# Optimization experiments

Hardware: AMD Instinct MI355X
Metric: run time of the kernel (lower is better)

## Reference

```python
import jax, jax.numpy as jnp
import numpy as np

N = 50000
E = 600000
DIN = 128
HID = 128
NG = 64


def _gat(x, src, dst, W, a_s, a_d, b, heads, dout, concat):
    # PyG GATConv (eval mode): per-head linear, edge attention logits,
    # segment softmax over destination nodes, weighted scatter-sum.
    n = x.shape[0]
    xp = (x @ W.T).reshape(n, heads, dout)                     # [n, H, D]
    e = jax.nn.leaky_relu(jnp.sum(xp * a_s, -1)[src] + jnp.sum(xp * a_d, -1)[dst], 0.2)  # [Etot, H]
    m = jax.ops.segment_max(e, dst, num_segments=n)
    ex = jnp.exp(e - m[dst])
    alpha = ex / jax.ops.segment_sum(ex, dst, num_segments=n)[dst]
    out = jax.ops.segment_sum(xp[src] * alpha[:, :, None], dst, num_segments=n)  # [n, H, D]
    out = out.reshape(n, heads * dout) if concat else out.mean(axis=1)
    return out + b


def _forward(x, edge_index, batch, Wi1, bi1, Wi2, bi2, Wg0, As0, Ad0, bg0, Wg1, As1, Ad1, bg1, Wg2, As2, Ad2, bg2, Wg3, As3, Ad3, bg3, We1, be1, We2, be2, Wc1, bc1, Wc2, bc2, Wc3, bc3):
    n = x.shape[0]
    loops = jnp.arange(n, dtype=edge_index.dtype)              # add_self_loops=True
    src = jnp.concatenate([edge_index[0], loops])
    dst = jnp.concatenate([edge_index[1], loops])
    # input_proj (dropout is a no-op in eval)
    h = jax.nn.relu(x @ Wi1.T + bi1) @ Wi2.T + bi2
    specs = [(Wg0, As0, Ad0, bg0, 8, 16, True),
             (Wg1, As1, Ad1, bg1, 8, 16, True),
             (Wg2, As2, Ad2, bg2, 8, 16, True),
             (Wg3, As3, Ad3, bg3, 1, 128, False)]
    for i, (W, a_s, a_d, b, hd, do, cc) in enumerate(specs):
        res = h
        h = jax.nn.elu(_gat(h, src, dst, W, a_s, a_d, b, hd, do, cc))
        if i > 0:
            h = h + res  # residual (dims always equal: 128)
    enh = h + (jax.nn.relu(h @ We1.T + be1) @ We2.T + be2)
    # per-graph mean / max / std (unbiased, ddof=1) pooling via segment reduces
    cnt = jax.ops.segment_sum(jnp.ones((n,), enh.dtype), batch, num_segments=NG)
    s = jax.ops.segment_sum(enh, batch, num_segments=NG)
    ss = jax.ops.segment_sum(enh * enh, batch, num_segments=NG)
    c = jnp.maximum(cnt, 1.0)[:, None]
    mean = s / c
    mx = jax.ops.segment_max(enh, batch, num_segments=NG)
    var = (ss - c * mean * mean) / jnp.maximum(cnt - 1.0, 1.0)[:, None]
    std = jnp.where(cnt[:, None] > 1.0, jnp.sqrt(jnp.maximum(var, 0.0)), 0.0)
    g = jnp.concatenate([mean, mx, std], axis=1)               # [NG, 3*HID]
    h1 = jax.nn.relu(g @ Wc1.T + bc1)
    h2 = jax.nn.relu(h1 @ Wc2.T + bc2)
    return h2 @ Wc3.T + bc3


def setup_inputs():
    ks = jax.random.split(jax.random.key(0), 32)

    def gl(k, o, i):
        return jax.random.normal(k, (o, i), jnp.float32) * jnp.sqrt(2.0 / (o + i))

    inp = {}
    inp["x"] = jax.random.normal(ks[0], (N, DIN), jnp.float32)
    inp["edge_index"] = jax.random.randint(ks[1], (2, E), 0, N, dtype=jnp.int32)
    inp["batch"] = jnp.sort(jax.random.randint(ks[2], (N,), 0, NG, dtype=jnp.int32))
    inp["Wi1"] = gl(ks[3], HID, DIN); inp["bi1"] = jnp.zeros((HID,), jnp.float32)
    inp["Wi2"] = gl(ks[4], HID, HID); inp["bi2"] = jnp.zeros((HID,), jnp.float32)
    for li in range(3):
        inp[f"Wg{li}"] = gl(ks[5 + li], HID, HID)
        inp[f"As{li}"] = jax.random.normal(ks[8 + li], (8, 16), jnp.float32) * 0.1
        inp[f"Ad{li}"] = jax.random.normal(ks[11 + li], (8, 16), jnp.float32) * 0.1
        inp[f"bg{li}"] = jnp.zeros((HID,), jnp.float32)
    inp["Wg3"] = gl(ks[14], HID, HID)
    inp["As3"] = jax.random.normal(ks[15], (1, HID), jnp.float32) * 0.1
    inp["Ad3"] = jax.random.normal(ks[16], (1, HID), jnp.float32) * 0.1
    inp["bg3"] = jnp.zeros((HID,), jnp.float32)
    inp["We1"] = gl(ks[17], HID, HID); inp["be1"] = jnp.zeros((HID,), jnp.float32)
    inp["We2"] = gl(ks[18], HID, HID); inp["be2"] = jnp.zeros((HID,), jnp.float32)
    inp["Wc1"] = gl(ks[19], HID, 3 * HID); inp["bc1"] = jnp.zeros((HID,), jnp.float32)
    inp["Wc2"] = gl(ks[20], HID // 2, HID); inp["bc2"] = jnp.zeros((HID // 2,), jnp.float32)
    inp["Wc3"] = gl(ks[21], 2, HID // 2); inp["bc3"] = jnp.zeros((2,), jnp.float32)
    return inp


def reference(x, edge_index, batch, Wi1, bi1, Wi2, bi2, Wg0, As0, Ad0, bg0, Wg1, As1, Ad1, bg1, Wg2, As2, Ad2, bg2, Wg3, As3, Ad3, bg3, We1, be1, We2, be2, Wc1, bc1, Wc2, bc2, Wc3, bc3):
    return _forward(x, edge_index, batch, Wi1, bi1, Wi2, bi2, Wg0, As0, Ad0, bg0, Wg1, As1, Ad1, bg1, Wg2, As2, Ad2, bg2, Wg3, As3, Ad3, bg3, We1, be1, We2, be2, Wc1, bc1, Wc2, bc2, Wc3, bc3)
```

## Files before the change

kernel.cpp:

```cpp
#include <hip/hip_runtime.h>
#include <hip/hip_fp16.h>
#include <cstddef>

typedef _Float16 f16;
typedef f16 f16x8 __attribute__((ext_vector_type(8)));
typedef float f32x4 __attribute__((ext_vector_type(4)));

__device__ __forceinline__ unsigned f2mono(float f){
  unsigned u = __float_as_uint(f);
  return (u & 0x80000000u) ? ~u : (u | 0x80000000u);
}
__device__ __forceinline__ float mono2f(unsigned u){
  return (u & 0x80000000u) ? __uint_as_float(u & 0x7fffffffu) : __uint_as_float(~u);
}

struct WPtrs { const float* w[8]; };
__global__ void k_wcast(WPtrs p, f16* __restrict__ Wh){
  int wi = blockIdx.y;
  const float* W = p.w[wi];
  f16* dst = Wh + (size_t)wi * 16384;
  int i = (blockIdx.x*256 + threadIdx.x) * 8;
  float4 v0 = *(const float4*)(W + i), v1 = *(const float4*)(W + i + 4);
  f16x8 h = {(f16)v0.x,(f16)v0.y,(f16)v0.z,(f16)v0.w,
             (f16)v1.x,(f16)v1.y,(f16)v1.z,(f16)v1.w};
  *(f16x8*)(dst + i) = h;
}

template<typename TIN, bool RES>
__global__ __launch_bounds__(256) void k_gemm2(
    const TIN* __restrict__ in, const f16* __restrict__ W1, const f16* __restrict__ W2,
    const float* __restrict__ b1, const float* __restrict__ b2,
    const float* __restrict__ res, float* __restrict__ outF, __half* __restrict__ outH, int n)
{
  constexpr int LDW = 130;
  __shared__ f16 Wl[128*LDW];
  __shared__ f16 Al[32*LDW];
  __shared__ f16 Ml[32*LDW];
  const int tid = threadIdx.x;
  const int r0 = blockIdx.x * 32;
#pragma unroll
  for (int i = 0; i < 8; i++){
    int u = tid + 256*i; int row = u >> 4, c8 = (u & 15) * 8;
    *(f16x8*)&Wl[row*LDW + c8] = *(const f16x8*)(W1 + (size_t)row*128 + c8);
  }
#pragma unroll
  for (int i = 0; i < 2; i++){
    int u = tid + 256*i; int row = u >> 4, c8 = (u & 15) * 8;
    int gr = r0 + row;
    f16x8 v = {};
    if (gr < n){
      if constexpr (__is_same(TIN, __half)){
        v = *(const f16x8*)((const f16*)in + (size_t)gr*128 + c8);
      } else {
        const float4* q = (const float4*)((const float*)in + (size_t)gr*128 + c8);
        float4 v0 = q[0], v1 = q[1];
        v = f16x8{(f16)v0.x,(f16)v0.y,(f16)v0.z,(f16)v0.w,
                  (f16)v1.x,(f16)v1.y,(f16)v1.z,(f16)v1.w};
      }
    }
    *(f16x8*)&Al[row*LDW + c8] = v;
  }
  __syncthreads();
  const int wv = tid >> 6, lane = tid & 63;
  const int l15 = lane & 15, quad = lane >> 4;
  f32x4 acc[2][2] = {};
  {
    const f16* Ab = &Al[l15*LDW + quad*8];
    const f16* Bb = &Wl[(wv*32 + l15)*LDW + quad*8];
#pragma unroll
    for (int kc = 0; kc < 4; kc++){
      f16x8 a0 = *(const f16x8*)(Ab + kc*32);
      f16x8 a1 = *(const f16x8*)(Ab + 16*LDW + kc*32);
#pragma unroll
      for (int nt = 0; nt < 2; nt++){
        f16x8 b = *(const f16x8*)(Bb + nt*16*LDW + kc*32);
        acc[0][nt] = __builtin_amdgcn_mfma_f32_16x16x32_f16(a0, b, acc[0][nt], 0, 0, 0);
        acc[1][nt] = __builtin_amdgcn_mfma_f32_16x16x32_f16(a1, b, acc[1][nt], 0, 0, 0);
      }
    }
  }
#pragma unroll
  for (int nt = 0; nt < 2; nt++){
    int col = wv*32 + nt*16 + l15;
    float bv = b1[col];
#pragma unroll
    for (int rh = 0; rh < 2; rh++)
#pragma unroll
      for (int reg = 0; reg < 4; reg++){
        int row = rh*16 + quad*4 + reg;
        Ml[row*LDW + col] = (f16)fmaxf(acc[rh][nt][reg] + bv, 0.f);
      }
  }
  __syncthreads();
#pragma unroll
  for (int i = 0; i < 8; i++){
    int u = tid + 256*i; int row = u >> 4, c8 = (u & 15) * 8;
    *(f16x8*)&Wl[row*LDW + c8] = *(const f16x8*)(W2 + (size_t)row*128 + c8);
  }
  __syncthreads();
  f32x4 acc2[2][2] = {};
  {
    const f16* Ab = &Ml[l15*LDW + quad*8];
    const f16* Bb = &Wl[(wv*32 + l15)*LDW + quad*8];
#pragma unroll
    for (int kc = 0; kc < 4; kc++){
      f16x8 a0 = *(const f16x8*)(Ab + kc*32);
      f16x8 a1 = *(const f16x8*)(Ab + 16*LDW + kc*32);
#pragma unroll
      for (int nt = 0; nt < 2; nt++){
        f16x8 b = *(const f16x8*)(Bb + nt*16*LDW + kc*32);
        acc2[0][nt] = __builtin_amdgcn_mfma_f32_16x16x32_f16(a0, b, acc2[0][nt], 0, 0, 0);
        acc2[1][nt] = __builtin_amdgcn_mfma_f32_16x16x32_f16(a1, b, acc2[1][nt], 0, 0, 0);
      }
    }
  }
  __syncthreads();
  float* Cf = (float*)Wl;
#pragma unroll
  for (int nt = 0; nt < 2; nt++){
    int col = wv*32 + nt*16 + l15;
    float bv = b2[col];
#pragma unroll
    for (int rh = 0; rh < 2; rh++)
#pragma unroll
      for (int reg = 0; reg < 4; reg++){
        int row = rh*16 + quad*4 + reg;
        Cf[row*132 + col] = acc2[rh][nt][reg] + bv;
      }
  }
  __syncthreads();
  if constexpr (RES){
#pragma unroll
    for (int i = 0; i < 4; i++){
      int u = tid + 256*i;
      int row = u >> 5, c4 = (u & 31) * 4;
      int gr = r0 + row;
      if (gr < n){
        float4 r4 = *(const float4*)(res + (size_t)gr*128 + c4);
        float4 v = *(float4*)&Cf[row*132 + c4];
        v.x += r4.x; v.y += r4.y; v.z += r4.z; v.w += r4.w;
        *(float4*)(outF + (size_t)gr*128 + c4) = v;
      }
    }
  } else {
#pragma unroll
    for (int i = 0; i < 2; i++){
      int u = tid + 256*i;
      int row = u >> 4, c8 = (u & 15) * 8;
      int gr = r0 + row;
      if (gr < n){
        float4 a = *(float4*)&Cf[row*132 + c8];
        float4 b = *(float4*)&Cf[row*132 + c8 + 4];
        f16x8 h = {(f16)a.x,(f16)a.y,(f16)a.z,(f16)a.w,
                   (f16)b.x,(f16)b.y,(f16)b.z,(f16)b.w};
        *(f16x8*)((f16*)outH + (size_t)gr*128 + c8) = h;
      }
    }
  }
}

template<int PREP>
__global__ __launch_bounds__(256) void k_gat_gemm(
    const __half* __restrict__ in, const f16* __restrict__ Wm,
    const float* __restrict__ As, const float* __restrict__ Ad,
    float* __restrict__ es, float* __restrict__ ed,
    __half* __restrict__ outH, int n)
{
  constexpr int LDW = 130;
  __shared__ f16 Wl[64*LDW];
  __shared__ f16 Al[32*LDW];
  const int tid = threadIdx.x;
  const int ch = blockIdx.x & 1;
  const int r0 = (blockIdx.x >> 1) * 32;
#pragma unroll
  for (int i = 0; i < 4; i++){
    int u = tid + 256*i; int row = u >> 4, c8 = (u & 15) * 8;
    *(f16x8*)&Wl[row*LDW + c8] = *(const f16x8*)(Wm + (size_t)(ch*64 + row)*128 + c8);
  }
#pragma unroll
  for (int i = 0; i < 2; i++){
    int u = tid + 256*i; int row = u >> 4, c8 = (u & 15) * 8;
    int gr = r0 + row;
    f16x8 v = {};
    if (gr < n) v = *(const f16x8*)((const f16*)in + (size_t)gr*128 + c8);
    *(f16x8*)&Al[row*LDW + c8] = v;
  }
  __syncthreads();
  const int wv = tid >> 6, lane = tid & 63;
  const int l15 = lane & 15, quad = lane >> 4;
  const int rh = wv & 1, cq = wv >> 1;
  f32x4 acc[2] = {};
  const f16* Ab = &Al[(rh*16 + l15)*LDW + quad*8];
  const f16* Bb = &Wl[(cq*32 + l15)*LDW + quad*8];
#pragma unroll
  for (int kc = 0; kc < 4; kc++){
    f16x8 a = *(const f16x8*)(Ab + kc*32);
#pragma unroll
    for (int nt = 0; nt < 2; nt++){
      f16x8 b = *(const f16x8*)(Bb + nt*16*LDW + kc*32);
      acc[nt] = __builtin_amdgcn_mfma_f32_16x16x32_f16(a, b, acc[nt], 0, 0, 0);
    }
  }
  if constexpr (PREP == 1){
#pragma unroll
    for (int nt = 0; nt < 2; nt++){
      int hh = ch*4 + cq*2 + nt;
      float as_ = As[hh*16 + l15], ad_ = Ad[hh*16 + l15];
#pragma unroll
      for (int reg = 0; reg < 4; reg++){
        float se = acc[nt][reg] * as_;
        float sd = acc[nt][reg] * ad_;
#pragma unroll
        for (int off = 1; off < 16; off <<= 1){
          se += __shfl_xor(se, off); sd += __shfl_xor(sd, off);
        }
        int gr = r0 + rh*16 + quad*4 + reg;
        if (l15 == 0 && gr < n){ es[gr*8 + hh] = se; ed[gr*8 + hh] = sd; }
      }
    }
  } else {
    float as_[2], ad_[2];
#pragma unroll
    for (int nt = 0; nt < 2; nt++){
      int col = ch*64 + cq*32 + nt*16 + l15;
      as_[nt] = As[col]; ad_[nt] = Ad[col];
    }
#pragma unroll
    for (int reg = 0; reg < 4; reg++){
      float se = acc[0][reg]*as_[0] + acc[1][reg]*as_[1];
      float sd = acc[0][reg]*ad_[0] + acc[1][reg]*ad_[1];
#pragma unroll
      for (int off = 1; off < 16; off <<= 1){
        se += __shfl_xor(se, off); sd += __shfl_xor(sd, off);
      }
      int gr = r0 + rh*16 + quad*4 + reg;
      if (l15 == 0 && gr < n){ atomicAdd(&es[gr], se); atomicAdd(&ed[gr], sd); }
    }
  }
  __syncthreads();
  f16* St = Al;
#pragma unroll
  for (int nt = 0; nt < 2; nt++){
    int c2 = cq*32 + nt*16 + l15;
#pragma unroll
    for (int reg = 0; reg < 4; reg++){
      int row = rh*16 + quad*4 + reg;
      St[row*72 + c2] = (f16)acc[nt][reg];
    }
  }
  __syncthreads();
  {
    int row = tid >> 3, c8 = (tid & 7) * 8;
    int gr = r0 + row;
    if (gr < n)
      *(f16x8*)((f16*)outH + (size_t)gr*128 + ch*64 + c8) = *(f16x8*)&St[row*72 + c8];
  }
}

__global__ void k_deg(const int* __restrict__ ei, int* __restrict__ deg, int E, int N){
  int t = blockIdx.x*blockDim.x + threadIdx.x;
  if (t >= E + N) return;
  int d = (t < E) ? ei[E + t] : (t - E);
  atomicAdd(&deg[d], 1);
}
__global__ void k_scan1(const int* __restrict__ deg, int* __restrict__ bsum, int N){
  __shared__ int sd[256];
  int i = blockIdx.x*256 + threadIdx.x;
  sd[threadIdx.x] = (i < N) ? deg[i] : 0;
  __syncthreads();
  for (int s = 128; s > 0; s >>= 1){
    if (threadIdx.x < s) sd[threadIdx.x] += sd[threadIdx.x + s];
    __syncthreads();
  }
  if (threadIdx.x == 0) bsum[blockIdx.x] = sd[0];
}
__global__ void k_scan2(const int* __restrict__ bsum, int* __restrict__ boff, int nb){
  __shared__ int sd[256];
  int t = threadIdx.x;
  int v = (t < nb) ? bsum[t] : 0;
  sd[t] = v;
  __syncthreads();
  for (int s = 1; s < 256; s <<= 1){
    int u = (t >= s) ? sd[t - s] : 0;
    __syncthreads();
    sd[t] += u;
    __syncthreads();
  }
  if (t < nb) boff[t] = sd[t] - v;
}
__global__ void k_scan3(const int* __restrict__ deg, const int* __restrict__ boff,
                        int* __restrict__ rowptr, int N){
  __shared__ int sd[256];
  int tid = threadIdx.x;
  int i = blockIdx.x*256 + tid;
  sd[tid] = (i < N) ? deg[i] : 0;
  __syncthreads();
  for (int s = 1; s < 256; s <<= 1){
    int t = (tid >= s) ? sd[tid - s] : 0;
    __syncthreads();
    sd[tid] += t;
    __syncthreads();
  }
  if (i < N) rowptr[i+1] = boff[blockIdx.x] + sd[tid];
  if (i == 0) rowptr[0] = 0;
}
__global__ void k_fill(const int* __restrict__ ei, const int* __restrict__ rowptr,
                       int* __restrict__ fil, int* __restrict__ csr, int E, int N){
  int t = blockIdx.x*blockDim.x + threadIdx.x;
  if (t >= E + N) return;
  int s, d;
  if (t < E){ s = ei[t]; d = ei[E + t]; } else { s = d = t - E; }
  int pos = rowptr[d] + atomicAdd(&fil[d], 1);
  csr[pos] = s;
}

template<int H, int D>
__global__ __launch_bounds__(256) void k_aggregate(
    const __half* __restrict__ xp, const float* __restrict__ es, const float* __restrict__ ed,
    const int* __restrict__ rowptr, const int* __restrict__ csr,
    const float* __restrict__ bg, const float* res,
    float* out, __half* __restrict__ outH, int N)
{
  int gw = (blockIdx.x*256 + threadIdx.x) >> 6;
  if (gw >= N) return;
  const int lane = threadIdx.x & 63;
  const int j0 = lane*2;
  const int h0 = (H == 8) ? (lane >> 3) : 0;
  const int k8 = lane & 7;
  int beg = rowptr[gw], end = rowptr[gw+1];
  float edv = ed[gw*H + h0];
  float den = 0.f, a0 = 0.f, a1 = 0.f;
  int idx = beg + k8; if (idx >= end) idx = end - 1;
  int sE = csr[idx];
  float ev = es[sE*H + h0];
  for (int t = beg; t < end; t += 8){
    int nb = end - t; if (nb > 8) nb = 8;
    int sE_c = sE; float ev_c = ev;
    int tn = t + 8;
    if (tn < end){
      int idxn = tn + k8; if (idxn >= end) idxn = end - 1;
      sE = csr[idxn];
      ev = es[sE*H + h0];
    }
    float e = ev_c + edv;
    e = e > 0.f ? e : 0.2f*e;
    if (k8 >= nb) e = -1e30f;
    float w = __expf(e);
    float wk[8]; int sk[8];
#pragma unroll
    for (int k = 0; k < 8; k++){
      wk[k] = __shfl(w, (h0 << 3) + k);
      sk[k] = __shfl(sE_c, k);
    }
    float2 f[8];
#pragma unroll
    for (int k = 0; k < 8; k++)
      f[k] = __half22float2(*(const __half2*)(xp + (size_t)sk[k]*128 + j0));
#pragma unroll
    for (int k = 0; k < 8; k++){
      den += wk[k]; a0 += wk[k]*f[k].x; a1 += wk[k]*f[k].y;
    }
  }
  float inv = 1.f / den;
  float o0 = a0*inv + bg[j0];
  float o1 = a1*inv + bg[j0+1];
  o0 = o0 > 0.f ? o0 : __expf(o0) - 1.f;
  o1 = o1 > 0.f ? o1 : __expf(o1) - 1.f;
  if (res){ o0 += res[(size_t)gw*128 + j0]; o1 += res[(size_t)gw*128 + j0 + 1]; }
  *(float2*)(out + (size_t)gw*128 + j0) = make_float2(o0, o1);
  *(__half2*)(outH + (size_t)gw*128 + j0) = __floats2half2_rn(o0, o1);
}

__global__ __launch_bounds__(128) void k_pool(const float* __restrict__ enh,
    const int* __restrict__ batch, float* __restrict__ Ps, float* __restrict__ Pss,
    unsigned* __restrict__ Pmx, float* __restrict__ Pcnt, int N)
{
  int tid = threadIdx.x;
  int n0 = blockIdx.x * 32;
  if (n0 >= N) return;
  int n1 = min(n0 + 32, N);
  int cur = batch[n0];
  float sum = 0.f, ssq = 0.f, mx = -1e30f, cnt = 0.f;
  auto flush = [&](int b){
    atomicAdd(&Ps[b*128 + tid], sum);
    atomicAdd(&Pss[b*128 + tid], ssq);
    atomicMax(&Pmx[b*128 + tid], f2mono(mx));
    if (tid == 0) atomicAdd(&Pcnt[b], cnt);
  };
  for (int i = n0; i < n1; i++){
    int b = batch[i];
    if (b != cur){ flush(cur); cur = b; sum = 0.f; ssq = 0.f; mx = -1e30f; cnt = 0.f; }
    float v = enh[(size_t)i*128 + tid];
    sum += v; ssq += v*v; mx = fmaxf(mx, v); cnt += 1.f;
  }
  flush(cur);
}

__global__ void k_poolcls(const float* __restrict__ Ps, const float* __restrict__ Pss,
    const unsigned* __restrict__ Pmx, const float* __restrict__ Pcnt,
    const float* __restrict__ Wc1, const float* __restrict__ bc1,
    const float* __restrict__ Wc2, const float* __restrict__ bc2,
    const float* __restrict__ Wc3, const float* __restrict__ bc3,
    float* __restrict__ out)
{
  __shared__ float gs[384];
  __shared__ float hs[128];
  __shared__ float h2[64];
  int b = blockIdx.x, j = threadIdx.x;
  float cnt = Pcnt[b];
  float c = fmaxf(cnt, 1.f);
  float mean = Ps[b*128 + j] / c;
  float var = (Pss[b*128 + j] - c*mean*mean) / fmaxf(cnt - 1.f, 1.f);
  float sd = (cnt > 1.f) ? sqrtf(fmaxf(var, 0.f)) : 0.f;
  gs[j] = mean; gs[128 + j] = mono2f(Pmx[b*128 + j]); gs[256 + j] = sd;
  __syncthreads();
  float acc = bc1[j];
  const float4* wr = (const float4*)(Wc1 + (size_t)j*384);
  for (int i = 0; i < 96; i++){
    float4 w = wr[i];
    acc += gs[i*4]*w.x + gs[i*4+1]*w.y + gs[i*4+2]*w.z + gs[i*4+3]*w.w;
  }
  hs[j] = fmaxf(acc, 0.f);
  __syncthreads();
  if (j < 64){
    float a2 = bc2[j];
    const float4* w2 = (const float4*)(Wc2 + (size_t)j*128);
    for (int i = 0; i < 32; i++){
      float4 w = w2[i];
      a2 += hs[i*4]*w.x + hs[i*4+1]*w.y + hs[i*4+2]*w.z + hs[i*4+3]*w.w;
    }
    h2[j] = fmaxf(a2, 0.f);
  }
  __syncthreads();
  if (j < 2){
    float a = bc3[j];
    for (int i = 0; i < 64; i++) a += h2[i] * Wc3[j*64 + i];
    out[b*2 + j] = a;
  }
}

extern "C" void kernel_launch(void* const* d_in, const int* in_sizes, int n_in,
                              void* d_out, int out_size, void* d_ws, size_t ws_size,
                              hipStream_t stream)
{
  const float* x    = (const float*)d_in[0];
  const int*  ei    = (const int*)d_in[1];
  const int*  batch = (const int*)d_in[2];
  const float* Wi1  = (const float*)d_in[3];  const float* bi1 = (const float*)d_in[4];
  const float* Wi2  = (const float*)d_in[5];  const float* bi2 = (const float*)d_in[6];
  const float* Wg[4]= {(const float*)d_in[7],(const float*)d_in[11],(const float*)d_in[15],(const float*)d_in[19]};
  const float* As[4]= {(const float*)d_in[8],(const float*)d_in[12],(const float*)d_in[16],(const float*)d_in[20]};
  const float* Ad[4]= {(const float*)d_in[9],(const float*)d_in[13],(const float*)d_in[17],(const float*)d_in[21]};
  const float* bg[4]= {(const float*)d_in[10],(const float*)d_in[14],(const float*)d_in[18],(const float*)d_in[22]};
  const float* We1  = (const float*)d_in[23]; const float* be1 = (const float*)d_in[24];
  const float* We2  = (const float*)d_in[25]; const float* be2 = (const float*)d_in[26];
  const float* Wc1  = (const float*)d_in[27]; const float* bc1 = (const float*)d_in[28];
  const float* Wc2  = (const float*)d_in[29]; const float* bc2 = (const float*)d_in[30];
  const float* Wc3  = (const float*)d_in[31]; const float* bc3 = (const float*)d_in[32];
  float* outp = (float*)d_out;

  const int N = in_sizes[2];
  const int E = in_sizes[1] / 2;
  const int Etot = E + N;

  float* base = (float*)d_ws;
  size_t off = 0;
  auto alloc = [&](size_t elems) -> float* {
    float* p = base + off;
    off += (elems + 3) & ~(size_t)3;
    return p;
  };
  float* A    = alloc((size_t)N * 128);
  __half* Xh  = (__half*)alloc((size_t)N * 64);
  __half* Ah  = (__half*)alloc((size_t)N * 64);
  f16* Wh     = (f16*)alloc(8 * 8192);
  float* es   = alloc((size_t)N * 8);
  float* ed   = alloc((size_t)N * 8);
  float* Ps   = alloc(64 * 128);
  float* Pss  = alloc(64 * 128);
  unsigned* Pmx = (unsigned*)alloc(64 * 128);
  float* Pcnt = alloc(64);
  int* deg    = (int*)alloc(N);
  int* fil    = (int*)alloc(N);
  float* es3  = alloc(N);
  float* ed3  = alloc(N);
  size_t zend = off;
  int* rowptr = (int*)alloc(N + 1);
  int* bsum   = (int*)alloc(512);
  int* boff   = (int*)alloc(512);
  int* csr    = (int*)alloc(Etot);
  (void)ws_size; (void)n_in; (void)out_size;

  (void)hipMemsetAsync(Ps, 0, (size_t)((base + zend) - Ps) * sizeof(float), stream);

  WPtrs wp;
  wp.w[0]=Wi1; wp.w[1]=Wi2; wp.w[2]=Wg[0]; wp.w[3]=Wg[1]; wp.w[4]=Wg[2]; wp.w[5]=Wg[3]; wp.w[6]=We1; wp.w[7]=We2;
  k_wcast<<<dim3(8, 8), 256, 0, stream>>>(wp, Wh);

  const int g2 = (N + 31) / 32;
  const int gtiles = 2 * g2;
  k_gemm2<float, false><<<g2, 256, 0, stream>>>(x, Wh + 0*16384, Wh + 1*16384, bi1, bi2,
                                                nullptr, nullptr, Ah, N);

  const int nb = (N + 255) / 256;
  k_deg  <<<(Etot + 255) / 256, 256, 0, stream>>>(ei, deg, E, N);
  k_scan1<<<nb, 256, 0, stream>>>(deg, bsum, N);
  k_scan2<<<1, 256, 0, stream>>>(bsum, boff, nb);
  k_scan3<<<nb, 256, 0, stream>>>(deg, boff, rowptr, N);
  k_fill <<<(Etot + 255) / 256, 256, 0, stream>>>(ei, rowptr, fil, csr, E, N);

  for (int l = 0; l < 4; l++){
    if (l < 3){
      k_gat_gemm<1><<<gtiles, 256, 0, stream>>>(Ah, Wh + (size_t)(2+l)*16384, As[l], Ad[l],
                                                es, ed, Xh, N);
      k_aggregate<8,16><<<(N + 3) / 4, 256, 0, stream>>>(Xh, es, ed, rowptr, csr, bg[l],
                                                         l > 0 ? A : nullptr, A, Ah, N);
    } else {
      k_gat_gemm<2><<<gtiles, 256, 0, stream>>>(Ah, Wh + 5*16384, As[3], Ad[3],
                                                es3, ed3, Xh, N);
      k_aggregate<1,128><<<(N + 3) / 4, 256, 0, stream>>>(Xh, es3, ed3, rowptr, csr, bg[3],
                                                          A, A, Ah, N);
    }
  }

  k_gemm2<__half, true><<<g2, 256, 0, stream>>>(Ah, Wh + 6*16384, Wh + 7*16384, be1, be2,
                                                A, A, nullptr, N);

  k_pool   <<<(N + 31) / 32, 128, 0, stream>>>(A, batch, Ps, Pss, Pmx, Pcnt, N);
  k_poolcls<<<64, 128, 0, stream>>>(Ps, Pss, Pmx, Pcnt, Wc1, bc1, Wc2, bc2, Wc3, bc3, outp);
}
```

Measured before the change: 567.9 us.

## Fuse pooling into enhancement GEMM and drop fp32 activation buffer

Per-graph pooling (sum, sum of squares, max, count) now runs inside the final two-layer GEMM epilogue, which removes the separate pool kernel and the fp32 write and read of the enhanced features. The residual path now uses the fp16 activation buffer in place of a separate fp32 copy. Aggregate kernels read the residual in fp16 and write only fp16 output. This roughly halves activation memory traffic but adds fp16 rounding to the residual stream, which can affect accuracy. Only 128 of 256 threads do the pooling in the epilogue.

After: 551.2 us. 1.03x faster.

```diff
diff --git a/kernel.cpp b/kernel.cpp
--- a/kernel.cpp
+++ b/kernel.cpp
@@ -26,16 +26,19 @@
   *(f16x8*)(dst + i) = h;
 }
 
-template<typename TIN, bool RES>
+template<typename TIN, int MODE>
 __global__ __launch_bounds__(256) void k_gemm2(
     const TIN* __restrict__ in, const f16* __restrict__ W1, const f16* __restrict__ W2,
     const float* __restrict__ b1, const float* __restrict__ b2,
-    const float* __restrict__ res, float* __restrict__ outF, __half* __restrict__ outH, int n)
+    const __half* __restrict__ resH, __half* __restrict__ outH,
+    const int* __restrict__ batch, float* __restrict__ Ps, float* __restrict__ Pss,
+    unsigned* __restrict__ Pmx, float* __restrict__ Pcnt, int n)
 {
   constexpr int LDW = 130;
   __shared__ f16 Wl[128*LDW];
   __shared__ f16 Al[32*LDW];
   __shared__ f16 Ml[32*LDW];
+  __shared__ int ib[32];
   const int tid = threadIdx.x;
   const int r0 = blockIdx.x * 32;
 #pragma unroll
@@ -128,21 +131,11 @@
         Cf[row*132 + col] = acc2[rh][nt][reg] + bv;
       }
   }
-  __syncthreads();
-  if constexpr (RES){
-#pragma unroll
-    for (int i = 0; i < 4; i++){
-      int u = tid + 256*i;
-      int row = u >> 5, c4 = (u & 31) * 4;
-      int gr = r0 + row;
-      if (gr < n){
-        float4 r4 = *(const float4*)(res + (size_t)gr*128 + c4);
-        float4 v = *(float4*)&Cf[row*132 + c4];
-        v.x += r4.x; v.y += r4.y; v.z += r4.z; v.w += r4.w;
-        *(float4*)(outF + (size_t)gr*128 + c4) = v;
-      }
-    }
-  } else {
+  if constexpr (MODE == 1){
+    if (tid < 32){ int gr = r0 + tid; ib[tid] = (gr < n) ? batch[gr] : -1; }
+  }
+  __syncthreads();
+  if constexpr (MODE == 0){
 #pragma unroll
     for (int i = 0; i < 2; i++){
       int u = tid + 256*i;
@@ -155,6 +148,25 @@
                    (f16)b.x,(f16)b.y,(f16)b.z,(f16)b.w};
         *(f16x8*)((f16*)outH + (size_t)gr*128 + c8) = h;
       }
+    }
+  } else {
+    if (tid < 128){
+      int j = tid;
+      float sum = 0.f, ssq = 0.f, mx = -1e30f, cnt = 0.f;
+      int cur = ib[0];
+      auto flush = [&](int b){
+        atomicAdd(&Ps[b*128 + j], sum);
+        atomicAdd(&Pss[b*128 + j], ssq);
+        atomicMax(&Pmx[b*128 + j], f2mono(mx));
+        if (j == 0) atomicAdd(&Pcnt[b], cnt);
+      };
+      for (int r = 0; r < 32; r++){
+        int b = ib[r]; if (b < 0) break;
+        float v = Cf[r*132 + j] + __half2float(resH[(size_t)(r0 + r)*128 + j]);
+        if (b != cur){ flush(cur); cur = b; sum = 0.f; ssq = 0.f; mx = -1e30f; cnt = 0.f; }
+        sum += v; ssq += v*v; mx = fmaxf(mx, v); cnt += 1.f;
+      }
+      if (cur >= 0) flush(cur);
     }
   }
 }
@@ -318,8 +330,8 @@
 __global__ __launch_bounds__(256) void k_aggregate(
     const __half* __restrict__ xp, const float* __restrict__ es, const float* __restrict__ ed,
     const int* __restrict__ rowptr, const int* __restrict__ csr,
-    const float* __restrict__ bg, const float* res,
-    float* out, __half* __restrict__ outH, int N)
+    const float* __restrict__ bg, const __half* __restrict__ resH,
+    __half* __restrict__ outH, int N)
 {
   int gw = (blockIdx.x*256 + threadIdx.x) >> 6;
   if (gw >= N) return;
@@ -366,34 +378,11 @@
   float o1 = a1*inv + bg[j0+1];
   o0 = o0 > 0.f ? o0 : __expf(o0) - 1.f;
   o1 = o1 > 0.f ? o1 : __expf(o1) - 1.f;
-  if (res){ o0 += res[(size_t)gw*128 + j0]; o1 += res[(size_t)gw*128 + j0 + 1]; }
-  *(float2*)(out + (size_t)gw*128 + j0) = make_float2(o0, o1);
+  if (resH){
+    float2 r = __half22float2(*(const __half2*)(resH + (size_t)gw*128 + j0));
+    o0 += r.x; o1 += r.y;
+  }
   *(__half2*)(outH + (size_t)gw*128 + j0) = __floats2half2_rn(o0, o1);
-}
-
-__global__ __launch_bounds__(128) void k_pool(const float* __restrict__ enh,
-    const int* __restrict__ batch, float* __restrict__ Ps, float* __restrict__ Pss,
-    unsigned* __restrict__ Pmx, float* __restrict__ Pcnt, int N)
-{
-  int tid = threadIdx.x;
-  int n0 = blockIdx.x * 32;
-  if (n0 >= N) return;
-  int n1 = min(n0 + 32, N);
-  int cur = batch[n0];
-  float sum = 0.f, ssq = 0.f, mx = -1e30f, cnt = 0.f;
-  auto flush = [&](int b){
-    atomicAdd(&Ps[b*128 + tid], sum);
-    atomicAdd(&Pss[b*128 + tid], ssq);
-    atomicMax(&Pmx[b*128 + tid], f2mono(mx));
-    if (tid == 0) atomicAdd(&Pcnt[b], cnt);
-  };
-  for (int i = n0; i < n1; i++){
-    int b = batch[i];
-    if (b != cur){ flush(cur); cur = b; sum = 0.f; ssq = 0.f; mx = -1e30f; cnt = 0.f; }
-    float v = enh[(size_t)i*128 + tid];
-    sum += v; ssq += v*v; mx = fmaxf(mx, v); cnt += 1.f;
-  }
-  flush(cur);
 }
 
 __global__ void k_poolcls(const float* __restrict__ Ps, const float* __restrict__ Pss,
@@ -470,7 +459,6 @@
     off += (elems + 3) & ~(size_t)3;
     return p;
   };
-  float* A    = alloc((size_t)N * 128);
   __half* Xh  = (__half*)alloc((size_t)N * 64);
   __half* Ah  = (__half*)alloc((size_t)N * 64);
   f16* Wh     = (f16*)alloc(8 * 8192);
@@ -499,8 +487,8 @@
 
   const int g2 = (N + 31) / 32;
   const int gtiles = 2 * g2;
-  k_gemm2<float, false><<<g2, 256, 0, stream>>>(x, Wh + 0*16384, Wh + 1*16384, bi1, bi2,
-                                                nullptr, nullptr, Ah, N);
+  k_gemm2<float, 0><<<g2, 256, 0, stream>>>(x, Wh + 0*16384, Wh + 1*16384, bi1, bi2,
+                                            nullptr, Ah, nullptr, nullptr, nullptr, nullptr, nullptr, N);
 
   const int nb = (N + 255) / 256;
   k_deg  <<<(Etot + 255) / 256, 256, 0, stream>>>(ei, deg, E, N);
@@ -514,18 +502,17 @@
       k_gat_gemm<1><<<gtiles, 256, 0, stream>>>(Ah, Wh + (size_t)(2+l)*16384, As[l], Ad[l],
                                                 es, ed, Xh, N);
       k_aggregate<8,16><<<(N + 3) / 4, 256, 0, stream>>>(Xh, es, ed, rowptr, csr, bg[l],
-                                                         l > 0 ? A : nullptr, A, Ah, N);
+                                                         l > 0 ? Ah : nullptr, Ah, N);
     } else {
       k_gat_gemm<2><<<gtiles, 256, 0, stream>>>(Ah, Wh + 5*16384, As[3], Ad[3],
                                                 es3, ed3, Xh, N);
       k_aggregate<1,128><<<(N + 3) / 4, 256, 0, stream>>>(Xh, es3, ed3, rowptr, csr, bg[3],
-                                                          A, A, Ah, N);
-    }
-  }
-
-  k_gemm2<__half, true><<<g2, 256, 0, stream>>>(Ah, Wh + 6*16384, Wh + 7*16384, be1, be2,
-                                                A, A, nullptr, N);
-
-  k_pool   <<<(N + 31) / 32, 128, 0, stream>>>(A, batch, Ps, Pss, Pmx, Pcnt, N);
+                                                          Ah, Ah, N);
+    }
+  }
+
+  k_gemm2<__half, 1><<<g2, 256, 0, stream>>>(Ah, Wh + 6*16384, Wh + 7*16384, be1, be2,
+                                             Ah, nullptr, batch, Ps, Pss, Pmx, Pcnt, N);
+
   k_poolcls<<<64, 128, 0, stream>>>(Ps, Pss, Pmx, Pcnt, Wc1, bc1, Wc2, bc2, Wc3, bc3, outp);
 }
```
